# Performance work log

Measured on AMD Instinct MI355X. Metric: run time of the kernel, lower is better.

## Reference

```python
import jax, jax.numpy as jnp
import numpy as np

N, DIN, DOUT = 8192, 256, 128
NEG_SLOPE = 0.01         # F.leaky_relu default
MASK_VAL = -9.0e15       # from the torch source


def setup_inputs() -> dict:
    key = jax.random.key(0)
    kx, kadj, kW, kbW, ka1, ka2, kba = jax.random.split(key, 7)
    x = jax.random.normal(kx, (N, DIN), dtype=jnp.float32)
    adj = jax.random.randint(kadj, (N, N), 0, 2, dtype=jnp.int32)
    # Linear W: input_dim -> output_dim
    W = jax.random.normal(kW, (DIN, DOUT), dtype=jnp.float32) * (1.0 / np.sqrt(DIN))
    bW = jax.random.normal(kbW, (DOUT,), dtype=jnp.float32) * 0.01
    # Linear a: 2*output_dim -> 1, split into the h_i part (a1) and h_j part (a2)
    a1 = jax.random.normal(ka1, (DOUT,), dtype=jnp.float32) * (1.0 / np.sqrt(2 * DOUT))
    a2 = jax.random.normal(ka2, (DOUT,), dtype=jnp.float32) * (1.0 / np.sqrt(2 * DOUT))
    ba = jax.random.normal(kba, (), dtype=jnp.float32) * 0.01
    return {"x": x, "adj": adj, "W": W, "bW": bW, "a1": a1, "a2": a2, "ba": ba}


def reference(x, adj, W, bW, a1, a2, ba):
    # h = W x + b  -> [N, DOUT]
    h = x @ W + bW
    # e[i,j] = leaky_relu(a . [h_i, h_j] + ba) = leaky_relu(a1.h_i + a2.h_j + ba)
    s_src = h @ a1            # [N]
    s_dst = h @ a2            # [N]
    e = s_src[:, None] + s_dst[None, :] + ba   # [N, N]
    e = jnp.where(e > 0, e, NEG_SLOPE * e)
    # mask non-edges, row softmax over neighbors j
    e = jnp.where(adj > 0, e, MASK_VAL)
    alpha = jax.nn.softmax(e, axis=1)          # [N, N]
    # dropout is identity in eval mode (dropout_rate=0)
    return alpha @ h                            # [N, DOUT]
```

## Files before the change

kernel.cpp:

```cpp
#include <hip/hip_runtime.h>
#include <hip/hip_bf16.h>


#define NN 8192
#define DIN 256
#define DOUT 128
#define LOG2E 1.4426950408889634f

typedef __attribute__((ext_vector_type(8))) short short8;
typedef __attribute__((ext_vector_type(4))) float floatx4;

__global__ void prep_wt(const float* __restrict__ W, __hip_bfloat16* __restrict__ WT) {
    int e = blockIdx.x * blockDim.x + threadIdx.x;
    if (e < DIN * DOUT) {
        int k = e >> 7;
        int d = e & 127;
        WT[d * DIN + k] = __float2bfloat16(W[e]);
    }
}

__global__ __launch_bounds__(256, 4) void gat_h(
    const float* __restrict__ x, const __hip_bfloat16* __restrict__ WT,
    const float* __restrict__ bW, const float* __restrict__ a1, const float* __restrict__ a2,
    __hip_bfloat16* __restrict__ hbB, float* __restrict__ s_src, float* __restrict__ s_dst) {
    int tid = threadIdx.x;
    int w = tid >> 6, lane = tid & 63;
    int lm = lane & 15, lq = lane >> 4;
    int i0 = blockIdx.x * 32;
    int r0 = (w >> 1) * 16;
    int c0 = (w & 1) * 64;

    __shared__ float s1s[32], s2s[32];
    if (tid < 32) { s1s[tid] = 0.f; s2s[tid] = 0.f; }
    __syncthreads();

    floatx4 acc[4] = {};
#pragma unroll
    for (int kk = 0; kk < DIN; kk += 32) {
        const float4* xp = (const float4*)&x[(size_t)(i0 + r0 + lm) * DIN + kk + lq * 8];
        float4 xa = xp[0], xb = xp[1];
        union { short8 v; __hip_bfloat16 h[8]; } af;
        af.h[0] = __float2bfloat16(xa.x); af.h[1] = __float2bfloat16(xa.y);
        af.h[2] = __float2bfloat16(xa.z); af.h[3] = __float2bfloat16(xa.w);
        af.h[4] = __float2bfloat16(xb.x); af.h[5] = __float2bfloat16(xb.y);
        af.h[6] = __float2bfloat16(xb.z); af.h[7] = __float2bfloat16(xb.w);
#pragma unroll
        for (int t = 0; t < 4; t++) {
            int d = c0 + 16 * t + lm;
            short8 bf = *(const short8*)&WT[(size_t)d * DIN + kk + lq * 8];
            acc[t] = __builtin_amdgcn_mfma_f32_16x16x32_bf16(af.v, bf, acc[t], 0, 0, 0);
        }
    }
    float s1[4] = {0.f, 0.f, 0.f, 0.f}, s2[4] = {0.f, 0.f, 0.f, 0.f};
#pragma unroll
    for (int t = 0; t < 4; t++) {
        int d = c0 + 16 * t + lm;
        int f = (c0 >> 4) + t;
        float A1 = a1[d], A2 = a2[d], B = bW[d];
#pragma unroll
        for (int r = 0; r < 4; r++) {
            int k = r0 + lq * 4 + r;
            float h = acc[t][r] + B;
            hbB[(size_t)blockIdx.x * 4096 + f * 512 + (k >> 3) * 128 + lm * 8 + (k & 7)] =
                __float2bfloat16(h);
            s1[r] += h * A1;
            s2[r] += h * A2;
        }
    }
#pragma unroll
    for (int r = 0; r < 4; r++) {
        for (int m = 1; m < 16; m <<= 1) {
            s1[r] += __shfl_xor(s1[r], m, 64);
            s2[r] += __shfl_xor(s2[r], m, 64);
        }
    }
    if (lm == 0) {
#pragma unroll
        for (int r = 0; r < 4; r++) {
            int row = r0 + lq * 4 + r;
            atomicAdd(&s1s[row], s1[r]);
            atomicAdd(&s2s[row], s2[r]);
        }
    }
    __syncthreads();
    if (tid < 32) {
        s_src[i0 + tid] = s1s[tid] * LOG2E;
        s_dst[i0 + tid] = s2s[tid] * LOG2E;
    }
}

template <int NJT>
__global__ void build_mask(const int* __restrict__ adj, unsigned char* __restrict__ mask) {
    size_t gid = (size_t)blockIdx.x * blockDim.x + threadIdx.x;
    const int4* a = (const int4*)(adj + gid * 8);
    int4 v0 = a[0], v1 = a[1];
    unsigned int b = 0;
    b |= (v0.x != 0) ? 1u : 0u;
    b |= (v0.y != 0) ? 2u : 0u;
    b |= (v0.z != 0) ? 4u : 0u;
    b |= (v0.w != 0) ? 8u : 0u;
    b |= (v1.x != 0) ? 16u : 0u;
    b |= (v1.y != 0) ? 32u : 0u;
    b |= (v1.z != 0) ? 64u : 0u;
    b |= (v1.w != 0) ? 128u : 0u;
    unsigned int g = (unsigned int)gid & (NJT * 4 - 1);
    size_t pos = (gid & ~(size_t)(NJT * 4 - 1)) | ((g & 3) * NJT + (g >> 2));
    mask[pos] = (unsigned char)b;
}

__device__ inline short8 make_pfrag(unsigned int cm, float ssi, float4 cd0, float4 cd1,
                                    floatx4* accd, const short8 ones) {
    float p[8];
    float e;
    e = ssi + cd0.x; e = fmaxf(e, 0.01f * e); p[0] = (cm & 1u)   ? __builtin_amdgcn_exp2f(e) : 0.f;
    e = ssi + cd0.y; e = fmaxf(e, 0.01f * e); p[1] = (cm & 2u)   ? __builtin_amdgcn_exp2f(e) : 0.f;
    e = ssi + cd0.z; e = fmaxf(e, 0.01f * e); p[2] = (cm & 4u)   ? __builtin_amdgcn_exp2f(e) : 0.f;
    e = ssi + cd0.w; e = fmaxf(e, 0.01f * e); p[3] = (cm & 8u)   ? __builtin_amdgcn_exp2f(e) : 0.f;
    e = ssi + cd1.x; e = fmaxf(e, 0.01f * e); p[4] = (cm & 16u)  ? __builtin_amdgcn_exp2f(e) : 0.f;
    e = ssi + cd1.y; e = fmaxf(e, 0.01f * e); p[5] = (cm & 32u)  ? __builtin_amdgcn_exp2f(e) : 0.f;
    e = ssi + cd1.z; e = fmaxf(e, 0.01f * e); p[6] = (cm & 64u)  ? __builtin_amdgcn_exp2f(e) : 0.f;
    e = ssi + cd1.w; e = fmaxf(e, 0.01f * e); p[7] = (cm & 128u) ? __builtin_amdgcn_exp2f(e) : 0.f;
    union { short8 v; __hip_bfloat162 q[4]; } af;
    af.q[0] = __float22bfloat162_rn(make_float2(p[0], p[1]));
    af.q[1] = __float22bfloat162_rn(make_float2(p[2], p[3]));
    af.q[2] = __float22bfloat162_rn(make_float2(p[4], p[5]));
    af.q[3] = __float22bfloat162_rn(make_float2(p[6], p[7]));
    *accd = __builtin_amdgcn_mfma_f32_16x16x32_bf16(af.v, ones, *accd, 0, 0, 0);
    return af.v;
}

template <int NJT>
__global__ __launch_bounds__(256, 1) void gat_attn(
    const unsigned char* __restrict__ mask, const float* __restrict__ s_src,
    const float* __restrict__ s_dst, const float* __restrict__ ba_p,
    const __hip_bfloat16* __restrict__ hbB,
    float* __restrict__ num, float* __restrict__ lpart) {
    int tid = threadIdx.x;
    int w = tid >> 6, lane = tid & 63;
    int lm = lane & 15, lq = lane >> 4;
    int b = blockIdx.x;
    int ib = b & 15;
    int jh = b >> 4;
    int i0 = ib * 512 + w * 128;
    int jb0 = jh * (NJT * 32);

    __shared__ float sdl[NJT * 32];

    union Mr { uint4 v[NJT / 16]; unsigned int u[NJT / 4]; };
    Mr mr[8];
    const unsigned char* mrow = mask + (size_t)(i0 + lm) * (NN / 8) + jh * (NJT * 4) + lq * NJT;
#pragma unroll
    for (int rg = 0; rg < 8; rg++)
#pragma unroll
        for (int q = 0; q < NJT / 16; q++)
            mr[rg].v[q] = ((const uint4*)(mrow + (size_t)rg * 16 * (NN / 8)))[q];

    float ba = ba_p[0] * LOG2E;
    float ssi[8];
#pragma unroll
    for (int rg = 0; rg < 8; rg++) ssi[rg] = s_src[i0 + rg * 16 + lm] + ba;

    const float* sdg = s_dst + jb0;
    for (int k = tid; k < NJT * 32; k += 256) sdl[k] = sdg[k];
    __syncthreads();

    const __hip_bfloat16* hb = hbB + ((size_t)(jh * NJT) * 8) * 512 + lane * 8;

    floatx4 acc[8][8] = {};
    floatx4 accd[8] = {};
    const short8 ones = { 0x3F80, 0x3F80, 0x3F80, 0x3F80, 0x3F80, 0x3F80, 0x3F80, 0x3F80 };

#pragma unroll
    for (int t = 0; t < NJT; t++) {
        float4 cd0 = *(const float4*)&sdl[t * 32 + lq * 8];
        float4 cd1 = *(const float4*)&sdl[t * 32 + lq * 8 + 4];
        short8 af[8];
#pragma unroll
        for (int rg = 0; rg < 8; rg++) {
            unsigned int cm = (mr[rg].u[t >> 2] >> ((t & 3) * 8)) & 0xFFu;
            af[rg] = make_pfrag(cm, ssi[rg], cd0, cd1, &accd[rg], ones);
        }
        const __hip_bfloat16* hbt = hb + (size_t)t * 8 * 512;
#pragma unroll
        for (int f = 0; f < 8; f++) {
            short8 bf = *(const short8*)(hbt + f * 512);
#pragma unroll
            for (int rg = 0; rg < 8; rg++)
                acc[rg][f] = __builtin_amdgcn_mfma_f32_16x16x32_bf16(af[rg], bf, acc[rg][f], 0, 0, 0);
        }
    }

    float* nb = num + ((size_t)jh * NN + i0) * DOUT;
#pragma unroll
    for (int rg = 0; rg < 8; rg++)
#pragma unroll
        for (int f = 0; f < 8; f++)
#pragma unroll
            for (int r = 0; r < 4; r++)
                __builtin_nontemporal_store(acc[rg][f][r],
                    &nb[(size_t)(rg * 16 + lq * 4 + r) * DOUT + f * 16 + lm]);
    if (lm == 0) {
#pragma unroll
        for (int rg = 0; rg < 8; rg++)
#pragma unroll
            for (int r = 0; r < 4; r++)
                lpart[(size_t)jh * NN + i0 + rg * 16 + lq * 4 + r] = accd[rg][r];
    }
}

__global__ void gat_combine(const float* __restrict__ num, const float* __restrict__ lpart,
                            float* __restrict__ out, int jsplit) {
    int gid = blockIdx.x * blockDim.x + threadIdx.x;
    int idx = gid * 4;
    int i = idx >> 7;
    float den = 0.f;
    for (int s = 0; s < jsplit; s++) den += lpart[(size_t)s * NN + i];
    float inv = 1.0f / den;
    floatx4 o = {0.f, 0.f, 0.f, 0.f};
    for (int s = 0; s < jsplit; s++) {
        floatx4 n = __builtin_nontemporal_load(
            (const floatx4*)&num[(size_t)s * NN * DOUT + idx]);
        o += n;
    }
    o *= inv;
    *(floatx4*)&out[idx] = o;
}

extern "C" void kernel_launch(void* const* d_in, const int* in_sizes, int n_in,
                              void* d_out, int out_size, void* d_ws, size_t ws_size,
                              hipStream_t stream) {
    const float* x  = (const float*)d_in[0];
    const int* adj  = (const int*)d_in[1];
    const float* W  = (const float*)d_in[2];
    const float* bW = (const float*)d_in[3];
    const float* a1 = (const float*)d_in[4];
    const float* a2 = (const float*)d_in[5];
    const float* ba = (const float*)d_in[6];
    float* out = (float*)d_out;

    char* ws = (char*)d_ws;
    __hip_bfloat16* hbB  = (__hip_bfloat16*)ws;
    __hip_bfloat16* WT   = (__hip_bfloat16*)(ws + 2097152);
    float* s_src         = (float*)(ws + 2162688);
    float* s_dst         = (float*)(ws + 2195456);
    float* lpart         = (float*)(ws + 2228224);
    unsigned char* mask  = (unsigned char*)(ws + 2752512);
    float* num           = (float*)(ws + 11141120);

    int jsplit = (ws_size >= 11141120 + (size_t)16 * NN * DOUT * 4) ? 16 : 8;

    if (jsplit == 16) build_mask<16><<<32768, 256, 0, stream>>>(adj, mask);
    else              build_mask<32><<<32768, 256, 0, stream>>>(adj, mask);
    prep_wt<<<128, 256, 0, stream>>>(W, WT);
    gat_h<<<256, 256, 0, stream>>>(x, WT, bW, a1, a2, hbB, s_src, s_dst);
    if (jsplit == 16)
        gat_attn<16><<<256, 256, 0, stream>>>(mask, s_src, s_dst, ba, hbB, num, lpart);
    else
        gat_attn<32><<<128, 256, 0, stream>>>(mask, s_src, s_dst, ba, hbB, num, lpart);
    gat_combine<<<1024, 256, 0, stream>>>(num, lpart, out, jsplit);
}
```

Baseline: 470.2 us.

## Restructure attention to split j across waves with in-block reduction, drop combine kernel

The attention kernel now gives each block 32 rows and splits the full j range across its 4 waves. h tiles are streamed into double-buffered LDS with global_load_lds while the previous tile is being computed. Partial numerators and denominators are reduced through shared memory and normalized in-kernel, which removes the large num/lpart workspace writes and the separate combine kernel. In exchange each wave holds far fewer rows (2 vs 8 row groups), so every h fragment is reused less and h traffic per block rises.

```diff
diff --git a/kernel.cpp b/kernel.cpp
--- a/kernel.cpp
+++ b/kernel.cpp
@@ -89,7 +89,6 @@
     }
 }
 
-template <int NJT>
 __global__ void build_mask(const int* __restrict__ adj, unsigned char* __restrict__ mask) {
     size_t gid = (size_t)blockIdx.x * blockDim.x + threadIdx.x;
     const int4* a = (const int4*)(adj + gid * 8);
@@ -103,8 +102,8 @@
     b |= (v1.y != 0) ? 32u : 0u;
     b |= (v1.z != 0) ? 64u : 0u;
     b |= (v1.w != 0) ? 128u : 0u;
-    unsigned int g = (unsigned int)gid & (NJT * 4 - 1);
-    size_t pos = (gid & ~(size_t)(NJT * 4 - 1)) | ((g & 3) * NJT + (g >> 2));
+    unsigned int g = (unsigned int)gid & 63u;
+    size_t pos = (gid & ~(size_t)63) | ((g & 3) * 16 + (g >> 2));
     mask[pos] = (unsigned char)b;
 }
 
@@ -129,101 +128,118 @@
     return af.v;
 }
 
-template <int NJT>
 __global__ __launch_bounds__(256, 1) void gat_attn(
     const unsigned char* __restrict__ mask, const float* __restrict__ s_src,
     const float* __restrict__ s_dst, const float* __restrict__ ba_p,
-    const __hip_bfloat16* __restrict__ hbB,
-    float* __restrict__ num, float* __restrict__ lpart) {
+    const __hip_bfloat16* __restrict__ hbB, float* __restrict__ out) {
     int tid = threadIdx.x;
     int w = tid >> 6, lane = tid & 63;
     int lm = lane & 15, lq = lane >> 4;
-    int b = blockIdx.x;
-    int ib = b & 15;
-    int jh = b >> 4;
-    int i0 = ib * 512 + w * 128;
-    int jb0 = jh * (NJT * 32);
-
-    __shared__ float sdl[NJT * 32];
-
-    union Mr { uint4 v[NJT / 16]; unsigned int u[NJT / 4]; };
-    Mr mr[8];
-    const unsigned char* mrow = mask + (size_t)(i0 + lm) * (NN / 8) + jh * (NJT * 4) + lq * NJT;
-#pragma unroll
-    for (int rg = 0; rg < 8; rg++)
-#pragma unroll
-        for (int q = 0; q < NJT / 16; q++)
-            mr[rg].v[q] = ((const uint4*)(mrow + (size_t)rg * 16 * (NN / 8)))[q];
+    int i0 = blockIdx.x * 32;
+
+    __shared__ short8 bbuf[4][2][512];
+    __shared__ float sdl[NN];
+    __shared__ float denr[4][32];
+
+    uint4 mr[2][4];
+#pragma unroll
+    for (int rg = 0; rg < 2; rg++)
+#pragma unroll
+        for (int tb = 0; tb < 4; tb++)
+            mr[rg][tb] = *(const uint4*)(mask + (size_t)(i0 + rg * 16 + lm) * (NN / 8)
+                                              + (w * 4 + tb) * 64 + lq * 16);
 
     float ba = ba_p[0] * LOG2E;
-    float ssi[8];
-#pragma unroll
-    for (int rg = 0; rg < 8; rg++) ssi[rg] = s_src[i0 + rg * 16 + lm] + ba;
-
-    const float* sdg = s_dst + jb0;
-    for (int k = tid; k < NJT * 32; k += 256) sdl[k] = sdg[k];
-    __syncthreads();
-
-    const __hip_bfloat16* hb = hbB + ((size_t)(jh * NJT) * 8) * 512 + lane * 8;
-
-    floatx4 acc[8][8] = {};
-    floatx4 accd[8] = {};
+    float ssi0 = s_src[i0 + lm] + ba;
+    float ssi1 = s_src[i0 + 16 + lm] + ba;
+
+    for (int k = tid; k < NN; k += 256) sdl[k] = s_dst[k];
+
+    const char* hbc = (const char*)hbB + (size_t)w * 64 * 8192;
+
+#define STAGEW(T, par)                                                                  \
+    do {                                                                                \
+        const char* g_ = hbc + (size_t)(T) * 8192 + lane * 16;                          \
+        char* l_ = (char*)&bbuf[w][par][0] + lane * 16;                                 \
+        _Pragma("unroll")                                                               \
+        for (int q_ = 0; q_ < 8; q_++)                                                  \
+            __builtin_amdgcn_global_load_lds(                                           \
+                (const __attribute__((address_space(1))) unsigned int*)(g_ + q_ * 1024),\
+                (__attribute__((address_space(3))) unsigned int*)(l_ + q_ * 1024),      \
+                16, 0, 0);                                                              \
+    } while (0)
+
+    STAGEW(0, 0);
+    __syncthreads();
+
+    floatx4 acc[2][8] = {};
+    floatx4 accd[2] = {};
     const short8 ones = { 0x3F80, 0x3F80, 0x3F80, 0x3F80, 0x3F80, 0x3F80, 0x3F80, 0x3F80 };
 
 #pragma unroll
-    for (int t = 0; t < NJT; t++) {
-        float4 cd0 = *(const float4*)&sdl[t * 32 + lq * 8];
-        float4 cd1 = *(const float4*)&sdl[t * 32 + lq * 8 + 4];
-        short8 af[8];
-#pragma unroll
-        for (int rg = 0; rg < 8; rg++) {
-            unsigned int cm = (mr[rg].u[t >> 2] >> ((t & 3) * 8)) & 0xFFu;
-            af[rg] = make_pfrag(cm, ssi[rg], cd0, cd1, &accd[rg], ones);
-        }
-        const __hip_bfloat16* hbt = hb + (size_t)t * 8 * 512;
-#pragma unroll
-        for (int f = 0; f < 8; f++) {
-            short8 bf = *(const short8*)(hbt + f * 512);
-#pragma unroll
-            for (int rg = 0; rg < 8; rg++)
-                acc[rg][f] = __builtin_amdgcn_mfma_f32_16x16x32_bf16(af[rg], bf, acc[rg][f], 0, 0, 0);
-        }
-    }
-
-    float* nb = num + ((size_t)jh * NN + i0) * DOUT;
-#pragma unroll
-    for (int rg = 0; rg < 8; rg++)
+    for (int tb = 0; tb < 4; tb++) {
+#pragma unroll
+        for (int ti = 0; ti < 16; ti++) {
+            const int t = tb * 16 + ti;
+            if (t < 63) {
+                STAGEW(t + 1, (t + 1) & 1);
+                asm volatile("s_waitcnt vmcnt(8)" ::: "memory");
+            } else {
+                asm volatile("s_waitcnt vmcnt(0)" ::: "memory");
+            }
+            __builtin_amdgcn_sched_barrier(0);
+
+            float4 cd0 = *(const float4*)&sdl[w * 2048 + t * 32 + lq * 8];
+            float4 cd1 = *(const float4*)&sdl[w * 2048 + t * 32 + lq * 8 + 4];
+            unsigned int u0 = ((const unsigned int*)&mr[0][tb])[ti >> 2];
+            unsigned int u1 = ((const unsigned int*)&mr[1][tb])[ti >> 2];
+            unsigned int cm0 = (u0 >> ((ti & 3) * 8)) & 0xFFu;
+            unsigned int cm1 = (u1 >> ((ti & 3) * 8)) & 0xFFu;
+            short8 af0 = make_pfrag(cm0, ssi0, cd0, cd1, &accd[0], ones);
+            short8 af1 = make_pfrag(cm1, ssi1, cd0, cd1, &accd[1], ones);
+#pragma unroll
+            for (int f = 0; f < 8; f++) {
+                short8 bf = bbuf[w][t & 1][f * 64 + lane];
+                acc[0][f] = __builtin_amdgcn_mfma_f32_16x16x32_bf16(af0, bf, acc[0][f], 0, 0, 0);
+                acc[1][f] = __builtin_amdgcn_mfma_f32_16x16x32_bf16(af1, bf, acc[1][f], 0, 0, 0);
+            }
+        }
+    }
+#undef STAGEW
+
+    __syncthreads();
+    float* red = (float*)bbuf;
+#pragma unroll
+    for (int rg = 0; rg < 2; rg++)
 #pragma unroll
         for (int f = 0; f < 8; f++)
 #pragma unroll
             for (int r = 0; r < 4; r++)
-                __builtin_nontemporal_store(acc[rg][f][r],
-                    &nb[(size_t)(rg * 16 + lq * 4 + r) * DOUT + f * 16 + lm]);
+                red[w * 4096 + (rg * 16 + lq * 4 + r) * 128 + f * 16 + lm] = acc[rg][f][r];
     if (lm == 0) {
 #pragma unroll
-        for (int rg = 0; rg < 8; rg++)
+        for (int rg = 0; rg < 2; rg++)
 #pragma unroll
             for (int r = 0; r < 4; r++)
-                lpart[(size_t)jh * NN + i0 + rg * 16 + lq * 4 + r] = accd[rg][r];
-    }
-}
-
-__global__ void gat_combine(const float* __restrict__ num, const float* __restrict__ lpart,
-                            float* __restrict__ out, int jsplit) {
-    int gid = blockIdx.x * blockDim.x + threadIdx.x;
-    int idx = gid * 4;
-    int i = idx >> 7;
-    float den = 0.f;
-    for (int s = 0; s < jsplit; s++) den += lpart[(size_t)s * NN + i];
+                denr[w][rg * 16 + lq * 4 + r] = accd[rg][r];
+    }
+    __syncthreads();
+
+    int row = tid >> 3;
+    int d0 = (tid & 7) * 16;
+    float den = denr[0][row] + denr[1][row] + denr[2][row] + denr[3][row];
     float inv = 1.0f / den;
-    floatx4 o = {0.f, 0.f, 0.f, 0.f};
-    for (int s = 0; s < jsplit; s++) {
-        floatx4 n = __builtin_nontemporal_load(
-            (const floatx4*)&num[(size_t)s * NN * DOUT + idx]);
-        o += n;
-    }
-    o *= inv;
-    *(floatx4*)&out[idx] = o;
+    float* ob = out + (size_t)(i0 + row) * DOUT + d0;
+#pragma unroll
+    for (int c = 0; c < 4; c++) {
+        int idx = row * 128 + d0 + c * 4;
+        floatx4 s = *(const floatx4*)&red[idx];
+        s += *(const floatx4*)&red[4096 + idx];
+        s += *(const floatx4*)&red[8192 + idx];
+        s += *(const floatx4*)&red[12288 + idx];
+        s *= inv;
+        *(floatx4*)(ob + c * 4) = s;
+    }
 }
 
 extern "C" void kernel_launch(void* const* d_in, const int* in_sizes, int n_in,
@@ -243,19 +259,10 @@
     __hip_bfloat16* WT   = (__hip_bfloat16*)(ws + 2097152);
     float* s_src         = (float*)(ws + 2162688);
     float* s_dst         = (float*)(ws + 2195456);
-    float* lpart         = (float*)(ws + 2228224);
     unsigned char* mask  = (unsigned char*)(ws + 2752512);
-    float* num           = (float*)(ws + 11141120);
-
-    int jsplit = (ws_size >= 11141120 + (size_t)16 * NN * DOUT * 4) ? 16 : 8;
-
-    if (jsplit == 16) build_mask<16><<<32768, 256, 0, stream>>>(adj, mask);
-    else              build_mask<32><<<32768, 256, 0, stream>>>(adj, mask);
+
+    build_mask<<<32768, 256, 0, stream>>>(adj, mask);
     prep_wt<<<128, 256, 0, stream>>>(W, WT);
     gat_h<<<256, 256, 0, stream>>>(x, WT, bW, a1, a2, hbB, s_src, s_dst);
-    if (jsplit == 16)
-        gat_attn<16><<<256, 256, 0, stream>>>(mask, s_src, s_dst, ba, hbB, num, lpart);
-    else
-        gat_attn<32><<<128, 256, 0, stream>>>(mask, s_src, s_dst, ba, hbB, num, lpart);
-    gat_combine<<<1024, 256, 0, stream>>>(num, lpart, out, jsplit);
-}
+    gat_attn<<<256, 256, 0, stream>>>(mask, s_src, s_dst, ba, hbB, out);
+}
```

Result: faster. 425.8 us (-9.4%).
